# Kernel optimization log

Hardware: AMD Instinct MI355X
Metric: run time of the kernel (lower is better)

## Reference

```python
import jax, jax.numpy as jnp
import numpy as np

N_W = 100000      # number of rows in `weights` (destination nodes)
N_SRC = 100000    # number of source nodes (rows in feat)
N_EDGES = 6400000 # flattened (source, destination) candidate pairs, avg degree 64
N_BAGS = 10000    # number of bags
FEAT_DIM = 2      # FEATURES_DIM in the original module


def setup_inputs() -> dict:
    key = jax.random.key(0)
    k1, k2, k3, k4, k5, k6 = jax.random.split(key, 6)
    return {
        "weights": jax.random.normal(k1, (N_W, 1), dtype=jnp.float32),
        "feat": jax.random.normal(k2, (N_SRC, FEAT_DIM), dtype=jnp.float32),
        "W_lin": jax.random.normal(k3, (1, FEAT_DIM), dtype=jnp.float32),  # LinearLayerAttri weight (no bias)
        "edge_src": jax.random.randint(k4, (N_EDGES,), 0, N_SRC, dtype=jnp.int32),
        "edge_dst": jax.random.randint(k5, (N_EDGES,), 0, N_W, dtype=jnp.int32),
        "bag_of_source": jax.random.randint(k6, (N_SRC,), 0, N_BAGS, dtype=jnp.int32),
        "num_bags": N_BAGS,
    }


def reference(weights, feat, W_lin, edge_src, edge_dst, bag_of_source, num_bags):
    # lin[src] = LinearLayerAttri(feat[src])  -> scalar per source node
    lin = (feat @ W_lin.T)[:, 0]                              # [N_SRC]
    # per-edge scaled weight: weights[dst] * lin[src]
    scaled = weights[edge_dst, 0] * lin[edge_src]             # [E]
    # per-source max over its destination candidates
    # (equals weights[argmax(scaled)] * lin[src] in the torch loop)
    per_src = jax.ops.segment_max(scaled, edge_src, num_segments=feat.shape[0])  # [N_SRC]
    # per-bag max over its source nodes
    bag_max = jax.ops.segment_max(per_src, bag_of_source, num_segments=num_bags)  # [N_BAGS]
    # torch init: max_weights starts at 0 and is only written when value > -10
    SENTINEL = -10.0
    max_weights = jnp.where(bag_max > SENTINEL, bag_max, 0.0)[:, None]  # [N_BAGS, 1]
    return (max_weights, per_src[:, None])
```

## Files before the change

### kernel.cpp

```cpp
#include <hip/hip_runtime.h>
#include <math.h>

typedef int   iv4 __attribute__((ext_vector_type(4)));
typedef float fv4 __attribute__((ext_vector_type(4)));

#define WQ_CAP      100352
#define ACC_CAP     50176
#define SGB_CAP     1568
#define PART_STRIDE 50176
#define NPART       256

__device__ __forceinline__ void atomicMaxF_dev(float* addr, float v) {
    if (v >= 0.0f) {
        atomicMax(reinterpret_cast<int*>(addr), __float_as_int(v));
    } else {
        atomicMin(reinterpret_cast<unsigned int*>(addr), __float_as_uint(v));
    }
}

__device__ __forceinline__ void ldsMaxI8(unsigned* wordPtr, int byteLane, int val) {
    const unsigned shift = byteLane * 8;
    const unsigned mask = 0xffu << shift;
    unsigned old = *((volatile unsigned*)wordPtr);
    while (true) {
        int cur = (int)(signed char)((old & mask) >> shift);
        if (val <= cur) return;
        unsigned neu = (old & ~mask) |
                       (((unsigned)(unsigned char)(signed char)val) << shift);
        unsigned prev = atomicCAS(wordPtr, old, neu);
        if (prev == old) return;
        old = prev;
    }
}

__global__ void prep_kernel(const float* __restrict__ feat,
                            const float* __restrict__ W_lin,
                            const float* __restrict__ w,
                            unsigned* __restrict__ sgb,
                            int* __restrict__ sc,
                            float* __restrict__ bagout,
                            int n_src, int n_w, int num_bags) {
    const int i = blockIdx.x * blockDim.x + threadIdx.x;
    if (i < num_bags) bagout[i] = -INFINITY;

    bool pred = false;
    if (i < n_src) {
        float2 f = *reinterpret_cast<const float2*>(feat + 2 * i);
        pred = fmaf(f.x, W_lin[0], f.y * W_lin[1]) >= 0.0f;
    }
    unsigned long long b = __ballot(pred);
    const int lane = threadIdx.x & 63;
    if (lane == 0) {
        const int nWords = (n_src + 31) >> 5;
        const int w0 = (i - lane) >> 5;
        if (w0 < nWords) sgb[w0] = (unsigned)b;
        if (w0 + 1 < nWords) sgb[w0 + 1] = (unsigned)(b >> 32);
    }

    float aw = (i < n_w) ? fabsf(w[i]) : 0.0f;
#pragma unroll
    for (int off = 32; off; off >>= 1) aw = fmaxf(aw, __shfl_down(aw, off, 64));
    if (lane == 0) atomicMax(sc, __float_as_int(aw));
}

__global__ __launch_bounds__(1024) void edge_part_kernel(
    const int* __restrict__ esrc, const int* __restrict__ edst,
    const float* __restrict__ w, const unsigned* __restrict__ sgb,
    const int* __restrict__ sc, unsigned char* __restrict__ parts,
    int n_w, int hb, int n_src, int nE) {
    __shared__ unsigned char lwq[WQ_CAP];
    __shared__ unsigned char lacc[ACC_CAP];
    __shared__ unsigned lsgb[SGB_CAP];

    const int tid = threadIdx.x;
    const int b = blockIdx.x;
    const int half = b >> 7;
    const int slice = b & 127;
    const int halfBase = half ? hb : 0;
    const int halfCnt = half ? (n_src - hb) : hb;

    const float maxab = __int_as_float(sc[0]);
    const float inv = (maxab > 0.0f) ? 127.0f / maxab : 0.0f;
    const int nw4 = n_w >> 2;
    for (int i = tid; i < nw4; i += 1024) {
        fv4 wv = reinterpret_cast<const fv4*>(w)[i];
        unsigned pk = 0;
#pragma unroll
        for (int k = 0; k < 4; ++k) {
            float q = rintf(wv[k] * inv);
            q = fminf(127.0f, fmaxf(-127.0f, q));
            pk |= ((unsigned)(unsigned char)(signed char)(int)q) << (8 * k);
        }
        reinterpret_cast<unsigned*>(lwq)[i] = pk;
    }
    for (int i = (nw4 << 2) + tid; i < n_w; i += 1024) {
        float q = rintf(w[i] * inv);
        q = fminf(127.0f, fmaxf(-127.0f, q));
        lwq[i] = (unsigned char)(signed char)(int)q;
    }
    const int accW = (halfCnt + 3) >> 2;
    for (int i = tid; i < accW; i += 1024)
        reinterpret_cast<unsigned*>(lacc)[i] = 0x80808080u;
    const int w0 = half ? (hb >> 5) : 0;
    const int myW = (halfCnt + 31) >> 5;
    for (int i = tid; i < myW; i += 1024) lsgb[i] = sgb[w0 + i];
    __syncthreads();

    const int nOct = nE >> 3;
    const int per = (nOct + 127) >> 7;
    const int lo = slice * per;
    const int hi = (lo + per < nOct) ? (lo + per) : nOct;

    for (int o = lo + tid; o < hi; o += 1024) {
        const int base = o << 3;
        iv4 sa = *reinterpret_cast<const iv4*>(esrc + base);
        iv4 sb = *reinterpret_cast<const iv4*>(esrc + base + 4);
        iv4 da = *reinterpret_cast<const iv4*>(edst + base);
        iv4 db = *reinterpret_cast<const iv4*>(edst + base + 4);
        int ss[8] = {sa.x, sa.y, sa.z, sa.w, sb.x, sb.y, sb.z, sb.w};
        int dd[8] = {da.x, da.y, da.z, da.w, db.x, db.y, db.z, db.w};
#pragma unroll
        for (int k = 0; k < 8; ++k) {
            unsigned u = (unsigned)(ss[k] - halfBase);
            if (u < (unsigned)halfCnt) {
                int wv = (int)(signed char)lwq[dd[k]];
                int sg = (lsgb[u >> 5] >> (u & 31)) & 1;
                int val = sg ? wv : -wv;
                int cur = (int)(signed char)lacc[u];
                if (val > cur)
                    ldsMaxI8(reinterpret_cast<unsigned*>(lacc) + (u >> 2),
                             u & 3, val);
            }
        }
    }
    if (slice == 127) {
        const int i = (nOct << 3) + tid;
        if (i < nE) {
            unsigned u = (unsigned)(esrc[i] - halfBase);
            if (u < (unsigned)halfCnt) {
                int wv = (int)(signed char)lwq[edst[i]];
                int sg = (lsgb[u >> 5] >> (u & 31)) & 1;
                int val = sg ? wv : -wv;
                int cur = (int)(signed char)lacc[u];
                if (val > cur)
                    ldsMaxI8(reinterpret_cast<unsigned*>(lacc) + (u >> 2),
                             u & 3, val);
            }
        }
    }
    __syncthreads();
    unsigned char* dst = parts + (size_t)b * PART_STRIDE;
    for (int i = tid; i < accW; i += 1024)
        reinterpret_cast<unsigned*>(dst)[i] =
            reinterpret_cast<unsigned*>(lacc)[i];
}

__global__ void merge_kernel(const unsigned char* __restrict__ parts,
                             const float* __restrict__ feat,
                             const float* __restrict__ W_lin,
                             const int* __restrict__ bag_of,
                             const int* __restrict__ sc,
                             float* __restrict__ out,
                             int hb, int n_src, int num_bags) {
    const int wordsPerHalf = ACC_CAP >> 2;
    const int t = blockIdx.x * blockDim.x + threadIdx.x;
    if (t >= 2 * wordsPerHalf) return;
    const int h = (t >= wordsPerHalf) ? 1 : 0;
    const int jw = t - h * wordsPerHalf;
    const int halfBase = h ? hb : 0;
    const int halfCnt = h ? (n_src - hb) : hb;
    if (jw * 4 >= halfCnt) return;

    int m0 = -128, m1 = -128, m2 = -128, m3 = -128;
    const unsigned char* base =
        parts + (size_t)(h * 128) * PART_STRIDE + (size_t)jw * 4;
    for (int k = 0; k < 128; ++k) {
        unsigned pw = *reinterpret_cast<const unsigned*>(
            base + (size_t)k * PART_STRIDE);
        int a0 = (int)(signed char)(pw & 0xff);
        int a1 = (int)(signed char)((pw >> 8) & 0xff);
        int a2 = (int)(signed char)((pw >> 16) & 0xff);
        int a3 = (int)(signed char)((pw >> 24) & 0xff);
        m0 = (a0 > m0) ? a0 : m0;
        m1 = (a1 > m1) ? a1 : m1;
        m2 = (a2 > m2) ? a2 : m2;
        m3 = (a3 > m3) ? a3 : m3;
    }
    const float step = __int_as_float(sc[0]) * (1.0f / 127.0f);
    const float w0 = W_lin[0], w1 = W_lin[1];
    int mm[4] = {m0, m1, m2, m3};
#pragma unroll
    for (int q = 0; q < 4; ++q) {
        const int u = jw * 4 + q;
        if (u < halfCnt) {
            const int s = halfBase + u;
            float2 f = *reinterpret_cast<const float2*>(feat + 2 * s);
            float lin = fmaf(f.x, w0, f.y * w1);
            float v = (mm[q] == -128) ? -INFINITY
                                      : fabsf(lin) * step * (float)mm[q] + 0.0f;
            out[num_bags + s] = v;
            atomicMaxF_dev(out + bag_of[s], v);
        }
    }
}

__global__ void finalize_kernel(float* __restrict__ bagbuf, int num_bags) {
    int i = blockIdx.x * blockDim.x + threadIdx.x;
    if (i < num_bags) {
        float v = bagbuf[i];
        bagbuf[i] = (v > -10.0f) ? v : 0.0f;
    }
}

__global__ void init_kernel(const float* __restrict__ feat,
                            const float* __restrict__ W_lin,
                            const float* __restrict__ w,
                            float2* __restrict__ snap, float* __restrict__ acc,
                            float* __restrict__ bagbuf, int* __restrict__ sc,
                            int n_src, int n_w, int num_bags) {
    int i = blockIdx.x * blockDim.x + threadIdx.x;
    if (i < n_src) {
        float2 f = *reinterpret_cast<const float2*>(feat + 2 * i);
        snap[i] = make_float2(fmaf(f.x, W_lin[0], f.y * W_lin[1]), -INFINITY);
        acc[i] = -INFINITY;
    }
    if (i < num_bags) bagbuf[i] = -INFINITY;
    float aw = (i < n_w) ? fabsf(w[i]) : 0.0f;
#pragma unroll
    for (int off = 32; off; off >>= 1) aw = fmaxf(aw, __shfl_down(aw, off, 64));
    if ((threadIdx.x & 63) == 0) atomicMax(sc, __float_as_int(aw));
}

template <bool QUANT>
__global__ void edge_fp32_kernel(const int* __restrict__ esrc,
                                 const int* __restrict__ edst,
                                 const float* __restrict__ weights,
                                 const float2* __restrict__ snap,
                                 float* __restrict__ acc,
                                 signed char* __restrict__ wq,
                                 const int* __restrict__ sc, int n_w,
                                 int octLo, int octHi, int nE, int isLast) {
    const int gsz = gridDim.x * blockDim.x;
    const int gid = blockIdx.x * blockDim.x + threadIdx.x;
    if (QUANT) {
        const float maxab = __int_as_float(sc[0]);
        const float inv = (maxab > 0.0f) ? 127.0f / maxab : 0.0f;
        for (int i = gid; i < n_w; i += gsz) {
            float q = rintf(weights[i] * inv);
            q = fminf(127.0f, fmaxf(-127.0f, q));
            wq[i] = (signed char)q;
        }
    }
    const int o = octLo + gid;
    if (o < octHi) {
        const int base = o << 3;
        iv4 sa = *reinterpret_cast<const iv4*>(esrc + base);
        iv4 sb = *reinterpret_cast<const iv4*>(esrc + base + 4);
        iv4 da = *reinterpret_cast<const iv4*>(edst + base);
        iv4 db = *reinterpret_cast<const iv4*>(edst + base + 4);
        int ss[8] = {sa.x, sa.y, sa.z, sa.w, sb.x, sb.y, sb.z, sb.w};
        int dd[8] = {da.x, da.y, da.z, da.w, db.x, db.y, db.z, db.w};
        float w[8];
        float2 p[8];
#pragma unroll
        for (int k = 0; k < 8; ++k) { w[k] = weights[dd[k]]; p[k] = snap[ss[k]]; }
#pragma unroll
        for (int k = 0; k < 8; ++k) {
            float v = w[k] * p[k].x + 0.0f;
            if (v >= p[k].y) atomicMaxF_dev(acc + ss[k], v);
        }
    }
    if (isLast) {
        const int done = (nE >> 3) << 3;
        const int i = done + gid;
        if (i < nE) {
            int s = esrc[i];
            float2 pp = snap[s];
            float v = weights[edst[i]] * pp.x + 0.0f;
            if (v >= pp.y) atomicMaxF_dev(acc + s, v);
        }
    }
}

__global__ void refresh_kernel(float2* __restrict__ snap,
                               const float* __restrict__ acc, int n_src) {
    int i = blockIdx.x * blockDim.x + threadIdx.x;
    if (i < n_src) snap[i].y = acc[i];
}

__global__ __launch_bounds__(1024) void edge_lds_kernel(
    const int* __restrict__ esrc, const int* __restrict__ edst,
    const signed char* __restrict__ wq, const int* __restrict__ sc,
    const float2* __restrict__ snap, float* __restrict__ acc, int n_w,
    int octLo, int octHi, int nE, int isLast) {
    __shared__ signed char lw[WQ_CAP];
    {
        const int nw16 = (n_w + 15) >> 4;
        const iv4* s16 = reinterpret_cast<const iv4*>(wq);
        iv4* d16 = reinterpret_cast<iv4*>(lw);
        for (int i = threadIdx.x; i < nw16; i += blockDim.x) d16[i] = s16[i];
    }
    const float step = __int_as_float(sc[0]) * (1.0f / 127.0f);
    __syncthreads();
    const int gsz = gridDim.x * blockDim.x;
    const int gid = blockIdx.x * blockDim.x + threadIdx.x;
    for (int o = octLo + gid; o < octHi; o += gsz) {
        const int base = o << 3;
        iv4 sa = *reinterpret_cast<const iv4*>(esrc + base);
        iv4 sb = *reinterpret_cast<const iv4*>(esrc + base + 4);
        iv4 da = *reinterpret_cast<const iv4*>(edst + base);
        iv4 db = *reinterpret_cast<const iv4*>(edst + base + 4);
        int ss[8] = {sa.x, sa.y, sa.z, sa.w, sb.x, sb.y, sb.z, sb.w};
        int dd[8] = {da.x, da.y, da.z, da.w, db.x, db.y, db.z, db.w};
        float wv[8];
        float2 p[8];
#pragma unroll
        for (int k = 0; k < 8; ++k) {
            wv[k] = (float)lw[dd[k]];
            p[k] = snap[ss[k]];
        }
#pragma unroll
        for (int k = 0; k < 8; ++k) {
            float v = wv[k] * step * p[k].x + 0.0f;
            if (v >= p[k].y) atomicMaxF_dev(acc + ss[k], v);
        }
    }
    if (isLast) {
        const int done = (nE >> 3) << 3;
        const int i = done + gid;
        if (i < nE) {
            int s = esrc[i];
            float2 pp = snap[s];
            float v = (float)lw[edst[i]] * step * pp.x + 0.0f;
            if (v >= pp.y) atomicMaxF_dev(acc + s, v);
        }
    }
}

__global__ void bag_kernel(const float* __restrict__ acc,
                           const int* __restrict__ bag_of,
                           float* __restrict__ per_src_out,
                           float* __restrict__ bagbuf, int n_src) {
    int i = blockIdx.x * blockDim.x + threadIdx.x;
    if (i < n_src) {
        float m = acc[i];
        per_src_out[i] = m;
        atomicMaxF_dev(bagbuf + bag_of[i], m);
    }
}


extern "C" void kernel_launch(void* const* d_in, const int* in_sizes, int n_in,
                              void* d_out, int out_size, void* d_ws,
                              size_t ws_size, hipStream_t stream) {
    const float* weights = (const float*)d_in[0];
    const float* feat    = (const float*)d_in[1];
    const float* W_lin   = (const float*)d_in[2];
    const int*   esrc    = (const int*)d_in[3];
    const int*   edst    = (const int*)d_in[4];
    const int*   bag_of  = (const int*)d_in[5];

    const int n_w      = in_sizes[0];
    const int n_src    = in_sizes[5];
    const int nE       = in_sizes[3];
    const int num_bags = out_size - n_src;

    float* out    = (float*)d_out;
    float* bagout = out;

    const int TB = 256;
    const int hb = ((n_src / 2) + 31) & ~31;
    const size_t needFast = (size_t)NPART * PART_STRIDE +
                            (((size_t)n_src + 31) / 32) * 4 + 64;
    const bool fastOk = (n_w <= WQ_CAP) && (hb <= ACC_CAP) &&
                        ((n_src - hb) <= ACC_CAP) && (n_src - hb) >= 0 &&
                        (ws_size >= needFast);

    if (fastOk) {
        unsigned char* parts = (unsigned char*)d_ws;
        unsigned* sgb = (unsigned*)(parts + (size_t)NPART * PART_STRIDE);
        int* sc = (int*)(sgb + ((size_t)n_src + 31) / 32);

        int n = (n_src > n_w) ? n_src : n_w;
        if (num_bags > n) n = num_bags;
        prep_kernel<<<(n + TB - 1) / TB, TB, 0, stream>>>(
            feat, W_lin, weights, sgb, sc, bagout, n_src, n_w, num_bags);

        edge_part_kernel<<<NPART, 1024, 0, stream>>>(
            esrc, edst, weights, sgb, sc, parts, n_w, hb, n_src, nE);

        const int mergeThreads = 2 * (ACC_CAP >> 2);
        merge_kernel<<<(mergeThreads + TB - 1) / TB, TB, 0, stream>>>(
            parts, feat, W_lin, bag_of, sc, out, hb, n_src, num_bags);

        finalize_kernel<<<(num_bags + TB - 1) / TB, TB, 0, stream>>>(
            bagout, num_bags);
        return;
    }

    float* per_src = out + num_bags;
    char* ws = (char*)d_ws;
    float2* snap = (float2*)ws;
    float* acc = (float*)(ws + (size_t)n_src * sizeof(float2));
    signed char* wq = (signed char*)(acc + n_src);
    int* sc = (int*)((char*)wq + (((size_t)n_w + 15) & ~(size_t)15));

    const int nOct = nE >> 3;
    const int c0 = nOct / 16;
    const int c1 = nOct / 4;
    const int refreshBlocks = (n_src + TB - 1) / TB;
    const bool useLds = (n_w + 15) <= WQ_CAP;

    {
        int n = (n_src > num_bags) ? n_src : num_bags;
        if (n_w > n) n = n_w;
        init_kernel<<<(n + TB - 1) / TB, TB, 0, stream>>>(
            feat, W_lin, weights, snap, acc, bagout, sc, n_src, n_w, num_bags);
    }
    if (c0 > 0) {
        int blocks = (c0 + TB - 1) / TB;
        if (useLds)
            edge_fp32_kernel<true><<<blocks, TB, 0, stream>>>(
                esrc, edst, weights, snap, acc, wq, sc, n_w, 0, c0, nE, 0);
        else
            edge_fp32_kernel<false><<<blocks, TB, 0, stream>>>(
                esrc, edst, weights, snap, acc, wq, sc, n_w, 0, c0, nE, 0);
        refresh_kernel<<<refreshBlocks, TB, 0, stream>>>(snap, acc, n_src);
    }
    if (c1 > c0) {
        int blocks = (c1 - c0 + TB - 1) / TB;
        edge_fp32_kernel<false><<<blocks, TB, 0, stream>>>(
            esrc, edst, weights, snap, acc, wq, sc, n_w, c0, c1, nE, 0);
        refresh_kernel<<<refreshBlocks, TB, 0, stream>>>(snap, acc, n_src);
    }
    if (useLds) {
        edge_lds_kernel<<<256, 1024, 0, stream>>>(
            esrc, edst, wq, sc, snap, acc, n_w, c1, nOct, nE, 1);
    } else {
        const int span = nOct - c1;
        int blocks = (span + TB - 1) / TB;
        if (blocks < 1) blocks = 1;
        edge_fp32_kernel<false><<<blocks, TB, 0, stream>>>(
            esrc, edst, weights, snap, acc, wq, sc, n_w, c1, nOct, nE, 1);
    }
    bag_kernel<<<(n_src + TB - 1) / TB, TB, 0, stream>>>(
        acc, bag_of, per_src, bagout, n_src);
    finalize_kernel<<<(num_bags + TB - 1) / TB, TB, 0, stream>>>(
        bagout, num_bags);
}
```

Baseline: 75.89 us.

## Fuse prep into edge kernel and split merge reduction across four lanes

Removes the separate prep kernel. Each edge-partition block now computes the max |weight| itself, builds its own sign bitmap from feat, and initializes the bag outputs, which saves a launch and a global round trip at the cost of redundant per-block reduction over the weights. The merge kernel spreads each 128-partition max reduction over four threads with shuffle combining, giving more parallelism and memory concurrency. It also drops the pre-check read of lacc before the LDS CAS max, so every in-range edge now goes through the CAS loop.

```diff
diff --git a/kernel.cpp b/kernel.cpp
--- a/kernel.cpp
+++ b/kernel.cpp
@@ -33,44 +33,16 @@
     }
 }
 
-__global__ void prep_kernel(const float* __restrict__ feat,
-                            const float* __restrict__ W_lin,
-                            const float* __restrict__ w,
-                            unsigned* __restrict__ sgb,
-                            int* __restrict__ sc,
-                            float* __restrict__ bagout,
-                            int n_src, int n_w, int num_bags) {
-    const int i = blockIdx.x * blockDim.x + threadIdx.x;
-    if (i < num_bags) bagout[i] = -INFINITY;
-
-    bool pred = false;
-    if (i < n_src) {
-        float2 f = *reinterpret_cast<const float2*>(feat + 2 * i);
-        pred = fmaf(f.x, W_lin[0], f.y * W_lin[1]) >= 0.0f;
-    }
-    unsigned long long b = __ballot(pred);
-    const int lane = threadIdx.x & 63;
-    if (lane == 0) {
-        const int nWords = (n_src + 31) >> 5;
-        const int w0 = (i - lane) >> 5;
-        if (w0 < nWords) sgb[w0] = (unsigned)b;
-        if (w0 + 1 < nWords) sgb[w0 + 1] = (unsigned)(b >> 32);
-    }
-
-    float aw = (i < n_w) ? fabsf(w[i]) : 0.0f;
-#pragma unroll
-    for (int off = 32; off; off >>= 1) aw = fmaxf(aw, __shfl_down(aw, off, 64));
-    if (lane == 0) atomicMax(sc, __float_as_int(aw));
-}
-
 __global__ __launch_bounds__(1024) void edge_part_kernel(
     const int* __restrict__ esrc, const int* __restrict__ edst,
-    const float* __restrict__ w, const unsigned* __restrict__ sgb,
-    const int* __restrict__ sc, unsigned char* __restrict__ parts,
-    int n_w, int hb, int n_src, int nE) {
+    const float* __restrict__ w, const float* __restrict__ feat,
+    const float* __restrict__ W_lin, unsigned char* __restrict__ parts,
+    float* __restrict__ bagout, float* __restrict__ scf,
+    int n_w, int hb, int n_src, int nE, int num_bags) {
     __shared__ unsigned char lwq[WQ_CAP];
     __shared__ unsigned char lacc[ACC_CAP];
     __shared__ unsigned lsgb[SGB_CAP];
+    __shared__ float red[16];
 
     const int tid = threadIdx.x;
     const int b = blockIdx.x;
@@ -79,8 +51,23 @@
     const int halfBase = half ? hb : 0;
     const int halfCnt = half ? (n_src - hb) : hb;
 
-    const float maxab = __int_as_float(sc[0]);
+    {
+        const int g = b * 1024 + tid;
+        if (g < num_bags) bagout[g] = -INFINITY;
+    }
+
+    float aw = 0.0f;
+    for (int i = tid; i < n_w; i += 1024) aw = fmaxf(aw, fabsf(w[i]));
+#pragma unroll
+    for (int off = 32; off; off >>= 1) aw = fmaxf(aw, __shfl_down(aw, off, 64));
+    if ((tid & 63) == 0) red[tid >> 6] = aw;
+    __syncthreads();
+    float maxab = red[0];
+#pragma unroll
+    for (int i = 1; i < 16; ++i) maxab = fmaxf(maxab, red[i]);
     const float inv = (maxab > 0.0f) ? 127.0f / maxab : 0.0f;
+    if (b == 0 && tid == 0) *scf = maxab;
+
     const int nw4 = n_w >> 2;
     for (int i = tid; i < nw4; i += 1024) {
         fv4 wv = reinterpret_cast<const fv4*>(w)[i];
@@ -101,9 +88,25 @@
     const int accW = (halfCnt + 3) >> 2;
     for (int i = tid; i < accW; i += 1024)
         reinterpret_cast<unsigned*>(lacc)[i] = 0x80808080u;
-    const int w0 = half ? (hb >> 5) : 0;
-    const int myW = (halfCnt + 31) >> 5;
-    for (int i = tid; i < myW; i += 1024) lsgb[i] = sgb[w0 + i];
+    {
+        const float w0 = W_lin[0], w1 = W_lin[1];
+        const int iters = (halfCnt + 1023) >> 10;
+        for (int it = 0; it < iters; ++it) {
+            const int u = it * 1024 + tid;
+            bool pred = false;
+            if (u < halfCnt) {
+                float2 f = *reinterpret_cast<const float2*>(
+                    feat + 2 * (size_t)(halfBase + u));
+                pred = fmaf(f.x, w0, f.y * w1) >= 0.0f;
+            }
+            unsigned long long bl = __ballot(pred);
+            if ((tid & 63) == 0) {
+                const int idx = it * 32 + (tid >> 6) * 2;
+                lsgb[idx] = (unsigned)bl;
+                lsgb[idx + 1] = (unsigned)(bl >> 32);
+            }
+        }
+    }
     __syncthreads();
 
     const int nOct = nE >> 3;
@@ -126,10 +129,8 @@
                 int wv = (int)(signed char)lwq[dd[k]];
                 int sg = (lsgb[u >> 5] >> (u & 31)) & 1;
                 int val = sg ? wv : -wv;
-                int cur = (int)(signed char)lacc[u];
-                if (val > cur)
-                    ldsMaxI8(reinterpret_cast<unsigned*>(lacc) + (u >> 2),
-                             u & 3, val);
+                ldsMaxI8(reinterpret_cast<unsigned*>(lacc) + (u >> 2),
+                         u & 3, val);
             }
         }
     }
@@ -141,10 +142,8 @@
                 int wv = (int)(signed char)lwq[edst[i]];
                 int sg = (lsgb[u >> 5] >> (u & 31)) & 1;
                 int val = sg ? wv : -wv;
-                int cur = (int)(signed char)lacc[u];
-                if (val > cur)
-                    ldsMaxI8(reinterpret_cast<unsigned*>(lacc) + (u >> 2),
-                             u & 3, val);
+                ldsMaxI8(reinterpret_cast<unsigned*>(lacc) + (u >> 2),
+                         u & 3, val);
             }
         }
     }
@@ -159,47 +158,65 @@
                              const float* __restrict__ feat,
                              const float* __restrict__ W_lin,
                              const int* __restrict__ bag_of,
-                             const int* __restrict__ sc,
+                             const float* __restrict__ scf,
                              float* __restrict__ out,
                              int hb, int n_src, int num_bags) {
     const int wordsPerHalf = ACC_CAP >> 2;
     const int t = blockIdx.x * blockDim.x + threadIdx.x;
-    if (t >= 2 * wordsPerHalf) return;
-    const int h = (t >= wordsPerHalf) ? 1 : 0;
-    const int jw = t - h * wordsPerHalf;
+    const int T = t >> 2;
+    const int q = t & 3;
+    if (T >= 2 * wordsPerHalf) return;
+    const int h = (T >= wordsPerHalf) ? 1 : 0;
+    const int jw = T - h * wordsPerHalf;
     const int halfBase = h ? hb : 0;
     const int halfCnt = h ? (n_src - hb) : hb;
-    if (jw * 4 >= halfCnt) return;
+    const bool live = (jw * 4 < halfCnt);
 
     int m0 = -128, m1 = -128, m2 = -128, m3 = -128;
-    const unsigned char* base =
-        parts + (size_t)(h * 128) * PART_STRIDE + (size_t)jw * 4;
-    for (int k = 0; k < 128; ++k) {
-        unsigned pw = *reinterpret_cast<const unsigned*>(
-            base + (size_t)k * PART_STRIDE);
-        int a0 = (int)(signed char)(pw & 0xff);
-        int a1 = (int)(signed char)((pw >> 8) & 0xff);
-        int a2 = (int)(signed char)((pw >> 16) & 0xff);
-        int a3 = (int)(signed char)((pw >> 24) & 0xff);
-        m0 = (a0 > m0) ? a0 : m0;
-        m1 = (a1 > m1) ? a1 : m1;
-        m2 = (a2 > m2) ? a2 : m2;
-        m3 = (a3 > m3) ? a3 : m3;
-    }
-    const float step = __int_as_float(sc[0]) * (1.0f / 127.0f);
-    const float w0 = W_lin[0], w1 = W_lin[1];
-    int mm[4] = {m0, m1, m2, m3};
-#pragma unroll
-    for (int q = 0; q < 4; ++q) {
-        const int u = jw * 4 + q;
-        if (u < halfCnt) {
-            const int s = halfBase + u;
-            float2 f = *reinterpret_cast<const float2*>(feat + 2 * s);
-            float lin = fmaf(f.x, w0, f.y * w1);
-            float v = (mm[q] == -128) ? -INFINITY
-                                      : fabsf(lin) * step * (float)mm[q] + 0.0f;
-            out[num_bags + s] = v;
-            atomicMaxF_dev(out + bag_of[s], v);
+    if (live) {
+        const unsigned char* base = parts +
+            (size_t)(h * 128 + q * 32) * PART_STRIDE + (size_t)jw * 4;
+        for (int k = 0; k < 32; ++k) {
+            unsigned pw = *reinterpret_cast<const unsigned*>(
+                base + (size_t)k * PART_STRIDE);
+            int a0 = (int)(signed char)(pw & 0xff);
+            int a1 = (int)(signed char)((pw >> 8) & 0xff);
+            int a2 = (int)(signed char)((pw >> 16) & 0xff);
+            int a3 = (int)(signed char)((pw >> 24) & 0xff);
+            m0 = (a0 > m0) ? a0 : m0;
+            m1 = (a1 > m1) ? a1 : m1;
+            m2 = (a2 > m2) ? a2 : m2;
+            m3 = (a3 > m3) ? a3 : m3;
+        }
+    }
+#pragma unroll
+    for (int d = 1; d <= 2; d <<= 1) {
+        int r0 = __shfl_xor(m0, d, 64);
+        int r1 = __shfl_xor(m1, d, 64);
+        int r2 = __shfl_xor(m2, d, 64);
+        int r3 = __shfl_xor(m3, d, 64);
+        m0 = (r0 > m0) ? r0 : m0;
+        m1 = (r1 > m1) ? r1 : m1;
+        m2 = (r2 > m2) ? r2 : m2;
+        m3 = (r3 > m3) ? r3 : m3;
+    }
+    if (q == 0 && live) {
+        const float step = (*scf) * (1.0f / 127.0f);
+        const float w0 = W_lin[0], w1 = W_lin[1];
+        int mm[4] = {m0, m1, m2, m3};
+#pragma unroll
+        for (int r = 0; r < 4; ++r) {
+            const int u = jw * 4 + r;
+            if (u < halfCnt) {
+                const int s = halfBase + u;
+                float2 f = *reinterpret_cast<const float2*>(feat + 2 * (size_t)s);
+                float lin = fmaf(f.x, w0, f.y * w1);
+                float v = (mm[r] == -128)
+                              ? -INFINITY
+                              : fabsf(lin) * step * (float)mm[r] + 0.0f;
+                out[num_bags + s] = v;
+                atomicMaxF_dev(out + bag_of[s], v);
+            }
         }
     }
 }
@@ -370,28 +387,22 @@
 
     const int TB = 256;
     const int hb = ((n_src / 2) + 31) & ~31;
-    const size_t needFast = (size_t)NPART * PART_STRIDE +
-                            (((size_t)n_src + 31) / 32) * 4 + 64;
+    const size_t needFast = (size_t)NPART * PART_STRIDE + 64;
     const bool fastOk = (n_w <= WQ_CAP) && (hb <= ACC_CAP) &&
-                        ((n_src - hb) <= ACC_CAP) && (n_src - hb) >= 0 &&
-                        (ws_size >= needFast);
+                        ((n_src - hb) <= ACC_CAP) && (n_src > hb) &&
+                        (ws_size >= needFast) && (num_bags <= NPART * 1024);
 
     if (fastOk) {
         unsigned char* parts = (unsigned char*)d_ws;
-        unsigned* sgb = (unsigned*)(parts + (size_t)NPART * PART_STRIDE);
-        int* sc = (int*)(sgb + ((size_t)n_src + 31) / 32);
-
-        int n = (n_src > n_w) ? n_src : n_w;
-        if (num_bags > n) n = num_bags;
-        prep_kernel<<<(n + TB - 1) / TB, TB, 0, stream>>>(
-            feat, W_lin, weights, sgb, sc, bagout, n_src, n_w, num_bags);
+        float* scf = (float*)(parts + (size_t)NPART * PART_STRIDE);
 
         edge_part_kernel<<<NPART, 1024, 0, stream>>>(
-            esrc, edst, weights, sgb, sc, parts, n_w, hb, n_src, nE);
-
-        const int mergeThreads = 2 * (ACC_CAP >> 2);
+            esrc, edst, weights, feat, W_lin, parts, bagout, scf,
+            n_w, hb, n_src, nE, num_bags);
+
+        const int mergeThreads = 2 * (ACC_CAP >> 2) * 4;
         merge_kernel<<<(mergeThreads + TB - 1) / TB, TB, 0, stream>>>(
-            parts, feat, W_lin, bag_of, sc, out, hb, n_src, num_bags);
+            parts, feat, W_lin, bag_of, scf, out, hb, n_src, num_bags);
 
         finalize_kernel<<<(num_bags + TB - 1) / TB, TB, 0, stream>>>(
             bagout, num_bags);
```

Result: faster. 72.94 us (-3.9%).

## Pre-quantize weights once, copy int8 into LDS, and split merge reduction across lanes

Applied to the files above, without the earlier changes.

A new quant_kernel quantizes weights to int8 once into workspace. Each of the 256 edge blocks then copies 100KB of int8 into LDS with 16-byte loads instead of re-reading 400KB of floats and quantizing them. The early-out check that skipped the LDS byte-max CAS when the value was not larger has been removed, so every edge now attempts the CAS. The merge kernel splits the 128-partition reduction across 4 lanes with a shuffle combine, which adds parallelism but costs one extra kernel launch.

```diff
diff --git a/kernel.cpp b/kernel.cpp
--- a/kernel.cpp
+++ b/kernel.cpp
@@ -45,7 +45,7 @@
 
     bool pred = false;
     if (i < n_src) {
-        float2 f = *reinterpret_cast<const float2*>(feat + 2 * i);
+        float2 f = *reinterpret_cast<const float2*>(feat + 2 * (size_t)i);
         pred = fmaf(f.x, W_lin[0], f.y * W_lin[1]) >= 0.0f;
     }
     unsigned long long b = __ballot(pred);
@@ -63,10 +63,23 @@
     if (lane == 0) atomicMax(sc, __float_as_int(aw));
 }
 
+__global__ void quant_kernel(const float* __restrict__ w,
+                             const int* __restrict__ sc,
+                             signed char* __restrict__ wq, int n_w) {
+    int i = blockIdx.x * blockDim.x + threadIdx.x;
+    if (i < n_w) {
+        float maxab = __int_as_float(sc[0]);
+        float inv = (maxab > 0.0f) ? 127.0f / maxab : 0.0f;
+        float q = rintf(w[i] * inv);
+        q = fminf(127.0f, fmaxf(-127.0f, q));
+        wq[i] = (signed char)q;
+    }
+}
+
 __global__ __launch_bounds__(1024) void edge_part_kernel(
     const int* __restrict__ esrc, const int* __restrict__ edst,
-    const float* __restrict__ w, const unsigned* __restrict__ sgb,
-    const int* __restrict__ sc, unsigned char* __restrict__ parts,
+    const signed char* __restrict__ wq, const unsigned* __restrict__ sgb,
+    unsigned char* __restrict__ parts,
     int n_w, int hb, int n_src, int nE) {
     __shared__ unsigned char lwq[WQ_CAP];
     __shared__ unsigned char lacc[ACC_CAP];
@@ -79,31 +92,20 @@
     const int halfBase = half ? hb : 0;
     const int halfCnt = half ? (n_src - hb) : hb;
 
-    const float maxab = __int_as_float(sc[0]);
-    const float inv = (maxab > 0.0f) ? 127.0f / maxab : 0.0f;
-    const int nw4 = n_w >> 2;
-    for (int i = tid; i < nw4; i += 1024) {
-        fv4 wv = reinterpret_cast<const fv4*>(w)[i];
-        unsigned pk = 0;
-#pragma unroll
-        for (int k = 0; k < 4; ++k) {
-            float q = rintf(wv[k] * inv);
-            q = fminf(127.0f, fmaxf(-127.0f, q));
-            pk |= ((unsigned)(unsigned char)(signed char)(int)q) << (8 * k);
-        }
-        reinterpret_cast<unsigned*>(lwq)[i] = pk;
-    }
-    for (int i = (nw4 << 2) + tid; i < n_w; i += 1024) {
-        float q = rintf(w[i] * inv);
-        q = fminf(127.0f, fmaxf(-127.0f, q));
-        lwq[i] = (unsigned char)(signed char)(int)q;
+    {
+        const int nw16 = (n_w + 15) >> 4;
+        const iv4* s16 = reinterpret_cast<const iv4*>(wq);
+        iv4* d16 = reinterpret_cast<iv4*>(lwq);
+        for (int i = tid; i < nw16; i += 1024) d16[i] = s16[i];
     }
     const int accW = (halfCnt + 3) >> 2;
     for (int i = tid; i < accW; i += 1024)
         reinterpret_cast<unsigned*>(lacc)[i] = 0x80808080u;
-    const int w0 = half ? (hb >> 5) : 0;
-    const int myW = (halfCnt + 31) >> 5;
-    for (int i = tid; i < myW; i += 1024) lsgb[i] = sgb[w0 + i];
+    {
+        const int w0 = half ? (hb >> 5) : 0;
+        const int myW = (halfCnt + 31) >> 5;
+        for (int i = tid; i < myW; i += 1024) lsgb[i] = sgb[w0 + i];
+    }
     __syncthreads();
 
     const int nOct = nE >> 3;
@@ -126,10 +128,8 @@
                 int wv = (int)(signed char)lwq[dd[k]];
                 int sg = (lsgb[u >> 5] >> (u & 31)) & 1;
                 int val = sg ? wv : -wv;
-                int cur = (int)(signed char)lacc[u];
-                if (val > cur)
-                    ldsMaxI8(reinterpret_cast<unsigned*>(lacc) + (u >> 2),
-                             u & 3, val);
+                ldsMaxI8(reinterpret_cast<unsigned*>(lacc) + (u >> 2),
+                         u & 3, val);
             }
         }
     }
@@ -141,10 +141,8 @@
                 int wv = (int)(signed char)lwq[edst[i]];
                 int sg = (lsgb[u >> 5] >> (u & 31)) & 1;
                 int val = sg ? wv : -wv;
-                int cur = (int)(signed char)lacc[u];
-                if (val > cur)
-                    ldsMaxI8(reinterpret_cast<unsigned*>(lacc) + (u >> 2),
-                             u & 3, val);
+                ldsMaxI8(reinterpret_cast<unsigned*>(lacc) + (u >> 2),
+                         u & 3, val);
             }
         }
     }
@@ -164,42 +162,60 @@
                              int hb, int n_src, int num_bags) {
     const int wordsPerHalf = ACC_CAP >> 2;
     const int t = blockIdx.x * blockDim.x + threadIdx.x;
-    if (t >= 2 * wordsPerHalf) return;
-    const int h = (t >= wordsPerHalf) ? 1 : 0;
-    const int jw = t - h * wordsPerHalf;
+    const int T = t >> 2;
+    const int q = t & 3;
+    if (T >= 2 * wordsPerHalf) return;
+    const int h = (T >= wordsPerHalf) ? 1 : 0;
+    const int jw = T - h * wordsPerHalf;
     const int halfBase = h ? hb : 0;
     const int halfCnt = h ? (n_src - hb) : hb;
-    if (jw * 4 >= halfCnt) return;
+    const bool live = (jw * 4 < halfCnt);
 
     int m0 = -128, m1 = -128, m2 = -128, m3 = -128;
-    const unsigned char* base =
-        parts + (size_t)(h * 128) * PART_STRIDE + (size_t)jw * 4;
-    for (int k = 0; k < 128; ++k) {
-        unsigned pw = *reinterpret_cast<const unsigned*>(
-            base + (size_t)k * PART_STRIDE);
-        int a0 = (int)(signed char)(pw & 0xff);
-        int a1 = (int)(signed char)((pw >> 8) & 0xff);
-        int a2 = (int)(signed char)((pw >> 16) & 0xff);
-        int a3 = (int)(signed char)((pw >> 24) & 0xff);
-        m0 = (a0 > m0) ? a0 : m0;
-        m1 = (a1 > m1) ? a1 : m1;
-        m2 = (a2 > m2) ? a2 : m2;
-        m3 = (a3 > m3) ? a3 : m3;
-    }
-    const float step = __int_as_float(sc[0]) * (1.0f / 127.0f);
-    const float w0 = W_lin[0], w1 = W_lin[1];
-    int mm[4] = {m0, m1, m2, m3};
-#pragma unroll
-    for (int q = 0; q < 4; ++q) {
-        const int u = jw * 4 + q;
-        if (u < halfCnt) {
-            const int s = halfBase + u;
-            float2 f = *reinterpret_cast<const float2*>(feat + 2 * s);
-            float lin = fmaf(f.x, w0, f.y * w1);
-            float v = (mm[q] == -128) ? -INFINITY
-                                      : fabsf(lin) * step * (float)mm[q] + 0.0f;
-            out[num_bags + s] = v;
-            atomicMaxF_dev(out + bag_of[s], v);
+    if (live) {
+        const unsigned char* base = parts +
+            (size_t)(h * 128 + q * 32) * PART_STRIDE + (size_t)jw * 4;
+        for (int k = 0; k < 32; ++k) {
+            unsigned pw = *reinterpret_cast<const unsigned*>(
+                base + (size_t)k * PART_STRIDE);
+            int a0 = (int)(signed char)(pw & 0xff);
+            int a1 = (int)(signed char)((pw >> 8) & 0xff);
+            int a2 = (int)(signed char)((pw >> 16) & 0xff);
+            int a3 = (int)(signed char)((pw >> 24) & 0xff);
+            m0 = (a0 > m0) ? a0 : m0;
+            m1 = (a1 > m1) ? a1 : m1;
+            m2 = (a2 > m2) ? a2 : m2;
+            m3 = (a3 > m3) ? a3 : m3;
+        }
+    }
+#pragma unroll
+    for (int d = 1; d <= 2; d <<= 1) {
+        int r0 = __shfl_xor(m0, d, 64);
+        int r1 = __shfl_xor(m1, d, 64);
+        int r2 = __shfl_xor(m2, d, 64);
+        int r3 = __shfl_xor(m3, d, 64);
+        m0 = (r0 > m0) ? r0 : m0;
+        m1 = (r1 > m1) ? r1 : m1;
+        m2 = (r2 > m2) ? r2 : m2;
+        m3 = (r3 > m3) ? r3 : m3;
+    }
+    if (q == 0 && live) {
+        const float step = __int_as_float(sc[0]) * (1.0f / 127.0f);
+        const float w0 = W_lin[0], w1 = W_lin[1];
+        int mm[4] = {m0, m1, m2, m3};
+#pragma unroll
+        for (int r = 0; r < 4; ++r) {
+            const int u = jw * 4 + r;
+            if (u < halfCnt) {
+                const int s = halfBase + u;
+                float2 f = *reinterpret_cast<const float2*>(feat + 2 * (size_t)s);
+                float lin = fmaf(f.x, w0, f.y * w1);
+                float v = (mm[r] == -128)
+                              ? -INFINITY
+                              : fabsf(lin) * step * (float)mm[r] + 0.0f;
+                out[num_bags + s] = v;
+                atomicMaxF_dev(out + bag_of[s], v);
+            }
         }
     }
 }
@@ -370,26 +386,32 @@
 
     const int TB = 256;
     const int hb = ((n_src / 2) + 31) & ~31;
+    const size_t sgbWords = ((size_t)n_src + 31) / 32;
     const size_t needFast = (size_t)NPART * PART_STRIDE +
-                            (((size_t)n_src + 31) / 32) * 4 + 64;
+                            (size_t)WQ_CAP +
+                            sgbWords * 4 + 64;
     const bool fastOk = (n_w <= WQ_CAP) && (hb <= ACC_CAP) &&
-                        ((n_src - hb) <= ACC_CAP) && (n_src - hb) >= 0 &&
+                        ((n_src - hb) <= ACC_CAP) && (n_src > hb) &&
                         (ws_size >= needFast);
 
     if (fastOk) {
         unsigned char* parts = (unsigned char*)d_ws;
-        unsigned* sgb = (unsigned*)(parts + (size_t)NPART * PART_STRIDE);
-        int* sc = (int*)(sgb + ((size_t)n_src + 31) / 32);
+        signed char* wq = (signed char*)(parts + (size_t)NPART * PART_STRIDE);
+        unsigned* sgb = (unsigned*)(wq + WQ_CAP);
+        int* sc = (int*)(sgb + sgbWords);
 
         int n = (n_src > n_w) ? n_src : n_w;
         if (num_bags > n) n = num_bags;
         prep_kernel<<<(n + TB - 1) / TB, TB, 0, stream>>>(
             feat, W_lin, weights, sgb, sc, bagout, n_src, n_w, num_bags);
 
+        quant_kernel<<<(n_w + TB - 1) / TB, TB, 0, stream>>>(
+            weights, sc, wq, n_w);
+
         edge_part_kernel<<<NPART, 1024, 0, stream>>>(
-            esrc, edst, weights, sgb, sc, parts, n_w, hb, n_src, nE);
-
-        const int mergeThreads = 2 * (ACC_CAP >> 2);
+            esrc, edst, wq, sgb, parts, n_w, hb, n_src, nE);
+
+        const int mergeThreads = 2 * (ACC_CAP >> 2) * 4;
         merge_kernel<<<(mergeThreads + TB - 1) / TB, TB, 0, stream>>>(
             parts, feat, W_lin, bag_of, sc, out, hb, n_src, num_bags);
 
```

New measurement: 61.01 us, median of 2. 1.24x faster.
